# Optimization experiments

Hardware: AMD Instinct MI355X
Metric: run time of the kernel (lower is better)

Reference implementation:

```python
import jax, jax.numpy as jnp
import numpy as np
import math

V = 32000      # vocab_size
D = 1024       # hidden_dims
T_MAX = 1024   # max_txt_len
L = 4          # n_layers
H = 8          # heads (fixed in CausalMHA)
HD = D // H
B, T = 2, 1024
EPS = 1e-5


def setup_inputs() -> dict:
    key = jax.random.key(0)
    ks = jax.random.split(key, 20)
    s = 0.02
    inp = {
        "x": jax.random.randint(ks[0], (B, T), 0, V, dtype=jnp.int64) if jax.config.read("jax_enable_x64") else jax.random.randint(ks[0], (B, T), 0, V, dtype=jnp.int32),
        "tok_emb": jax.random.normal(ks[1], (V, D), jnp.float32) * s,
        "pos_emb": jax.random.normal(ks[2], (1, T_MAX, D), jnp.float32) * s,
        "ln1_g": jnp.ones((L, D), jnp.float32),
        "ln1_b": jnp.zeros((L, D), jnp.float32),
        "wqkv": jax.random.normal(ks[3], (L, D, 3 * D), jnp.float32) * s,
        "bqkv": jnp.zeros((L, 3 * D), jnp.float32),
        "wo": jax.random.normal(ks[4], (L, D, D), jnp.float32) * s,
        "bo": jnp.zeros((L, D), jnp.float32),
        "ln2_g": jnp.ones((L, D), jnp.float32),
        "ln2_b": jnp.zeros((L, D), jnp.float32),
        "wfc": jax.random.normal(ks[5], (L, D, 4 * D), jnp.float32) * s,   # no bias
        "wfc2": jax.random.normal(ks[6], (L, 4 * D, D), jnp.float32) * s,  # no bias
        "fn_g": jnp.ones((D,), jnp.float32),
        "fn_b": jnp.zeros((D,), jnp.float32),
        "wout": jax.random.normal(ks[7], (D, V), jnp.float32) * s,
        "bout": jnp.zeros((V,), jnp.float32),
    }
    return inp


def _ln(x, g, b):
    mu = jnp.mean(x, axis=-1, keepdims=True)
    var = jnp.var(x, axis=-1, keepdims=True)
    return (x - mu) * jax.lax.rsqrt(var + EPS) * g + b


def _attn(xn, wqkv_l, bqkv_l, wo_l, bo_l):
    Bb, Tt, _ = xn.shape
    qkv = xn @ wqkv_l + bqkv_l                      # [B,T,3D]
    q, k, v = jnp.split(qkv, 3, axis=-1)
    q = q.reshape(Bb, Tt, H, HD)
    k = k.reshape(Bb, Tt, H, HD)
    v = v.reshape(Bb, Tt, H, HD)
    scores = jnp.einsum("bqhd,bkhd->bhqk", q, k) / math.sqrt(HD)
    mask = jnp.triu(jnp.ones((Tt, Tt), bool), k=1)   # True above diagonal
    scores = jnp.where(mask, jnp.float32(-jnp.inf), scores)
    att = jax.nn.softmax(scores, axis=-1)
    out = jnp.einsum("bhqk,bkhd->bqhd", att, v).reshape(Bb, Tt, D)
    return out @ wo_l + bo_l


def reference(x, tok_emb, pos_emb, ln1_g, ln1_b, wqkv, bqkv, wo, bo,
              ln2_g, ln2_b, wfc, wfc2, fn_g, fn_b, wout, bout):
    Tt = x.shape[1]
    h = tok_emb[x] + pos_emb[:, :Tt, :]              # [B,T,D]
    for i in range(L):
        h = h + _attn(_ln(h, ln1_g[i], ln1_b[i]), wqkv[i], bqkv[i], wo[i], bo[i])
        hn = _ln(h, ln2_g[i], ln2_b[i])
        h = h + jax.nn.gelu(hn @ wfc[i], approximate=False) @ wfc2[i]
    h = _ln(h, fn_g, fn_b)
    return h @ wout + bout                           # [B,T,V] logits
```

## Files before the change

### kernel.cpp

```cpp
#include <hip/hip_runtime.h>
#include <math.h>
#include <stdint.h>

#define D_  1024
#define T_  1024
#define H_  8
#define HD_ 128
#define L_  4
#define V_  32000
#define M_  2048

typedef __attribute__((ext_vector_type(4))) float f32x4;
typedef __attribute__((ext_vector_type(4))) short s16x4;
typedef __attribute__((ext_vector_type(8))) short s16x8;
typedef unsigned short u16;

__device__ __forceinline__ u16 f2bf(float f) {
  union { float f; uint32_t u; } c; c.f = f;
  uint32_t r = c.u + 0x7fffu + ((c.u >> 16) & 1u);
  return (u16)(r >> 16);
}
__device__ __forceinline__ float bf2f(u16 h) {
  union { uint32_t u; float f; } c; c.u = ((uint32_t)h) << 16;
  return c.f;
}
__device__ __forceinline__ float gelu_f(float x) {
  return 0.5f * x * (1.0f + erff(x * 0.70710678118654752f));
}

__device__ __forceinline__ void gload16(const u16* g, u16* l) {
  __builtin_amdgcn_global_load_lds(
      (const __attribute__((address_space(1))) void*)(uintptr_t)g,
      (__attribute__((address_space(3))) void*)(uint32_t)(uintptr_t)l,
      16, 0, 0);
}

__device__ __forceinline__ void convT_f32_tile(const float* __restrict__ in,
                                               u16* __restrict__ out,
                                               int ldin, int ldout,
                                               int c0, int r0,
                                               u16 (*tile)[72])
{
  const int t = threadIdx.x;
  const int rr = t >> 2, cs = (t & 3) << 4;
  u16 tmp[16];
  const float* p = in + (size_t)(r0 + rr) * ldin + c0 + cs;
#pragma unroll
  for (int q = 0; q < 4; ++q) {
    f32x4 v = *(const f32x4*)(p + q * 4);
#pragma unroll
    for (int j = 0; j < 4; ++j) tmp[q * 4 + j] = f2bf(v[j]);
  }
  *(s16x8*)&tile[rr][cs]     = *(const s16x8*)tmp;
  *(s16x8*)&tile[rr][cs + 8] = *(const s16x8*)(tmp + 8);
  __syncthreads();
  const int cr = t >> 2, rs = (t & 3) << 4;
  u16 o[16];
#pragma unroll
  for (int j = 0; j < 16; ++j) o[j] = tile[rs + j][cr];
  u16* op = out + (size_t)(c0 + cr) * ldout + r0 + rs;
  *(s16x8*)op       = *(const s16x8*)o;
  *(s16x8*)(op + 8) = *(const s16x8*)(o + 8);
}

__device__ __forceinline__
void ln_row_body(int row, float* __restrict__ hbuf, const float* __restrict__ P,
                 const float* __restrict__ g, const float* __restrict__ b,
                 u16* __restrict__ y, int red, float* red_s)
{
  const int tid = threadIdx.x;
  const size_t i = (size_t)row * D_ + tid * 4;
  f32x4 v = *(const f32x4*)&hbuf[i];
  if (red) {
#pragma unroll
    for (int zp = 0; zp < 4; ++zp) {
      f32x4 p = *(const f32x4*)&P[(size_t)zp * M_ * D_ + i];
      v[0] += p[0]; v[1] += p[1]; v[2] += p[2]; v[3] += p[3];
    }
    *(f32x4*)&hbuf[i] = v;
  }
  float s  = v[0] + v[1] + v[2] + v[3];
  float s2 = v[0]*v[0] + v[1]*v[1] + v[2]*v[2] + v[3]*v[3];
#pragma unroll
  for (int off = 32; off > 0; off >>= 1) {
    s  += __shfl_xor(s, off);
    s2 += __shfl_xor(s2, off);
  }
  if ((tid & 63) == 0) { red_s[tid >> 6] = s; red_s[4 + (tid >> 6)] = s2; }
  __syncthreads();
  s  = red_s[0] + red_s[1] + red_s[2] + red_s[3];
  s2 = red_s[4] + red_s[5] + red_s[6] + red_s[7];
  const float mean = s * (1.0f / D_);
  const float var  = s2 * (1.0f / D_) - mean * mean;
  const float rs   = rsqrtf(var + 1e-5f);
  f32x4 gg = *(const f32x4*)&g[tid * 4];
  f32x4 bb = *(const f32x4*)&b[tid * 4];
  u16 o[4];
#pragma unroll
  for (int j = 0; j < 4; ++j) o[j] = f2bf((v[j] - mean) * rs * gg[j] + bb[j]);
  *(s16x4*)&y[i] = *(const s16x4*)o;
}

__global__ __launch_bounds__(256)
void convT_bf16(const u16* __restrict__ in, u16* __restrict__ out,
                int ldin, int ldout, long inZ, long outZ)
{
  __shared__ __align__(16) u16 tile[64][72];
  const int c0 = blockIdx.x << 6, r0 = blockIdx.y << 6;
  const int t = threadIdx.x;
  const int rr = t >> 2, cs = (t & 3) << 4;
  const u16* p = in + (size_t)blockIdx.z * inZ + (size_t)(r0 + rr) * ldin + c0 + cs;
  s16x8 v0 = *(const s16x8*)(p);
  s16x8 v1 = *(const s16x8*)(p + 8);
  *(s16x8*)&tile[rr][cs]     = v0;
  *(s16x8*)&tile[rr][cs + 8] = v1;
  __syncthreads();
  const int cr = t >> 2, rs = (t & 3) << 4;
  u16 o[16];
#pragma unroll
  for (int j = 0; j < 16; ++j) o[j] = tile[rs + j][cr];
  u16* op = out + (size_t)blockIdx.z * outZ + (size_t)(c0 + cr) * ldout + r0 + rs;
  *(s16x8*)op       = *(const s16x8*)o;
  *(s16x8*)(op + 8) = *(const s16x8*)(o + 8);
}

__global__ __launch_bounds__(256)
void conv4ln_kernel(const float* __restrict__ wqkv_l, const float* __restrict__ wo_l,
                    const float* __restrict__ wfc_l, const float* __restrict__ wfc2_l,
                    u16* __restrict__ Wq, u16* __restrict__ Wo,
                    u16* __restrict__ Wf1, u16* __restrict__ Wf2,
                    float* __restrict__ hbuf, const float* __restrict__ P,
                    const float* __restrict__ g, const float* __restrict__ b,
                    u16* __restrict__ y, int red)
{
  __shared__ __align__(16) u16 tile[64][72];
  int f = blockIdx.x;
  if (f < 2048) { ln_row_body(f, hbuf, P, g, b, y, red, (float*)tile); return; }
  f -= 2048;
  if (f < 768) {
    convT_f32_tile(wqkv_l, Wq, 3 * D_, D_, (f % 48) << 6, (f / 48) << 6, tile);
  } else if (f < 1024) {
    f -= 768;
    convT_f32_tile(wo_l, Wo, D_, D_, (f & 15) << 6, (f >> 4) << 6, tile);
  } else if (f < 2048) {
    f -= 1024;
    convT_f32_tile(wfc_l, Wf1, 4 * D_, D_, (f & 63) << 6, (f >> 6) << 6, tile);
  } else {
    f -= 2048;
    convT_f32_tile(wfc2_l, Wf2, D_, 4 * D_, (f & 15) << 6, (f >> 4) << 6, tile);
  }
}

__global__ __launch_bounds__(256)
void convwout_ln(const float* __restrict__ wout, u16* __restrict__ WoutT,
                 float* __restrict__ hbuf, const float* __restrict__ P,
                 const float* __restrict__ g, const float* __restrict__ b,
                 u16* __restrict__ y)
{
  __shared__ __align__(16) u16 tile[64][72];
  int f = blockIdx.x;
  if (f < 2048) { ln_row_body(f, hbuf, P, g, b, y, 1, (float*)tile); return; }
  f -= 2048;
  convT_f32_tile(wout, WoutT, V_, D_, (f % 500) << 6, (f / 500) << 6, tile);
}

template<int TM, int ACT, int BIAS, int OUT>
__device__ __forceinline__
void gemm2_body(const u16* __restrict__ A, const u16* __restrict__ Bw,
                const float* __restrict__ bias, const float* __restrict__ res,
                void* __restrict__ Cv,
                int K, int lda, int ldb, int ldc, float scale,
                int bx, int by)
{
  constexpr int WN  = (TM == 128) ? 2 : 4;
  constexpr int WNW = 128 / WN;
  constexpr int NJ  = WNW / 16;
  constexpr int AR  = TM / 64;

  const int m0 = bx * TM, n0 = by * 128;
  const int ktiles = K >> 5;

  __shared__ __align__(16) u16 As[2][TM * 32];
  __shared__ __align__(16) u16 Bs[2][128 * 32];

  const int tid = threadIdx.x, lane = tid & 63, wave = tid >> 6;
  const int wm = wave / WN, wn = wave % WN;
  const int l15 = lane & 15, l4 = lane >> 4;
  const int srow = lane >> 2, scol = (lane & 3) << 3;

  f32x4 acc[4][NJ];
  const f32x4 z4 = {0.f, 0.f, 0.f, 0.f};
#pragma unroll
  for (int i = 0; i < 4; ++i)
#pragma unroll
    for (int j = 0; j < NJ; ++j) acc[i][j] = z4;

  auto stage = [&](int kt, int buf) {
    const int kc = (kt << 5) + scol;
#pragma unroll
    for (int r = 0; r < AR; ++r) {
      const int row = r * 64 + wave * 16;
      gload16(A + (size_t)(m0 + row + srow) * lda + kc, &As[buf][row * 32]);
    }
#pragma unroll
    for (int r = 0; r < 2; ++r) {
      const int row = r * 64 + wave * 16;
      gload16(Bw + (size_t)(n0 + row + srow) * ldb + kc, &Bs[buf][row * 32]);
    }
  };

  stage(0, 0);
  __syncthreads();

  for (int kt = 0; kt < ktiles; ++kt) {
    const int buf = kt & 1;
    if (kt + 1 < ktiles) stage(kt + 1, buf ^ 1);
    const u16* ap = &As[buf][(wm * 64 + l15) * 32 + (l4 << 3)];
    const u16* bp = &Bs[buf][(wn * WNW + l15) * 32 + (l4 << 3)];
    s16x8 af[4], bf[NJ];
#pragma unroll
    for (int i = 0; i < 4; ++i) af[i] = *(const s16x8*)(ap + i * (16 * 32));
#pragma unroll
    for (int j = 0; j < NJ; ++j) bf[j] = *(const s16x8*)(bp + j * (16 * 32));
#pragma unroll
    for (int i = 0; i < 4; ++i)
#pragma unroll
      for (int j = 0; j < NJ; ++j)
        acc[i][j] = __builtin_amdgcn_mfma_f32_16x16x32_bf16(af[i], bf[j], acc[i][j], 0, 0, 0);
    __syncthreads();
  }

  float* Cf = (float*)Cv;
  u16*   Ch = (u16*)Cv;
#pragma unroll
  for (int i = 0; i < 4; ++i) {
    const int row0 = m0 + wm * 64 + i * 16 + l4 * 4;
#pragma unroll
    for (int j = 0; j < NJ; ++j) {
      const int col = n0 + wn * WNW + j * 16 + l15;
      const float bv = BIAS ? bias[col] : 0.0f;
#pragma unroll
      for (int r = 0; r < 4; ++r) {
        float v = acc[i][j][r] * scale + bv;
        if (ACT) v = gelu_f(v);
        const size_t idx = (size_t)(row0 + r) * ldc + col;
        if (OUT == 0)      Ch[idx] = f2bf(v);
        else if (OUT == 1) Cf[idx] = v;
        else               Cf[idx] = v + res[idx];
      }
    }
  }
}

__device__ __forceinline__ int2 swz2d() {
  const int gx = gridDim.x, gy = gridDim.y;
  int flat = blockIdx.y * gx + blockIdx.x;
  const int nwg = gx * gy;
  int swz = (flat & 7) * (nwg >> 3) + (flat >> 3);
  return make_int2(swz % gx, swz / gx);
}

__global__ __launch_bounds__(256)
void gemm_qkv(const u16* A, const u16* Bw, const float* bias, void* Cv) {
  int2 b = swz2d();
  gemm2_body<128, 0, 1, 0>(A, Bw, bias, nullptr, Cv, D_, D_, D_, 3 * D_, 1.0f, b.x, b.y);
}
__global__ __launch_bounds__(256)
void gemm_wo(const u16* A, const u16* Bw, const float* bias, const float* res,
             void* Cv) {
  int2 b = swz2d();
  gemm2_body<64, 0, 1, 2>(A, Bw, bias, res, Cv, D_, D_, D_, D_, 1.0f, b.x, b.y);
}

template<int OUT, int ACT>
__device__ __forceinline__
void gemm8n_body(const u16* __restrict__ A, int lda,
                 const u16* __restrict__ Bw, int ldb,
                 void* __restrict__ Cv, int ldc, int bx, int by)
{
  const int m0 = bx << 8, n0 = by << 7;

  __shared__ __align__(16) u16 lds[49152];

  const int tid = threadIdx.x, lane = tid & 63, wave = tid >> 6;
  const int wm = wave >> 1, wn = wave & 1;
  const int l15 = lane & 15, l4 = lane >> 4;

  f32x4 acc[4][4];
  const f32x4 z4 = {0.f, 0.f, 0.f, 0.f};
#pragma unroll
  for (int i = 0; i < 4; ++i)
#pragma unroll
    for (int j = 0; j < 4; ++j) acc[i][j] = z4;

  auto stgA = [&](int buf, int kt, int kh) {
    kt = (kt < 15) ? kt : 15;
    const int slot = buf * 24576 + kh * 8192;
#pragma unroll
    for (int r = 0; r < 2; ++r) {
      const int u = r * 512 + (wave << 6) + lane;
      const int rw = u >> 2, ks = u & 3;
      const int ksw = ks ^ ((rw >> 1) & 3);
      gload16(A + (size_t)(m0 + rw) * lda + (kt << 6) + (kh << 5) + (ksw << 3),
              &lds[slot + r * 4096 + (wave << 9)]);
    }
  };
  auto stgB = [&](int buf, int kt, int kh) {
    kt = (kt < 15) ? kt : 15;
    const int slot = buf * 24576 + 16384 + kh * 4096;
    const int u = (wave << 6) + lane;
    const int rw = u >> 2, ks = u & 3;
    const int ksw = ks ^ ((rw >> 1) & 3);
    gload16(Bw + (size_t)(n0 + rw) * ldb + (kt << 6) + (kh << 5) + (ksw << 3),
            &lds[slot + (wave << 9)]);
  };

  s16x8 af[4], bfr[4];

#define LDABN(bb, kk)                                                         \
  {                                                                           \
    _Pragma("unroll") for (int f = 0; f < 4; ++f) {                           \
      const int rw = wm * 64 + f * 16 + l15;                                  \
      af[f] = *(const s16x8*)&lds[(bb) + (kk) * 8192 + rw * 32 +              \
                                  ((l4 ^ ((rw >> 1) & 3)) << 3)];             \
    }                                                                         \
    _Pragma("unroll") for (int f = 0; f < 4; ++f) {                           \
      const int rn = wn * 64 + f * 16 + l15;                                  \
      bfr[f] = *(const s16x8*)&lds[(bb) + 16384 + (kk) * 4096 + rn * 32 +     \
                                   ((l4 ^ ((rn >> 1) & 3)) << 3)];            \
    }                                                                         \
  }
#define MFMAN()                                                               \
  {                                                                           \
    __builtin_amdgcn_s_barrier();                                             \
    asm volatile("s_waitcnt lgkmcnt(0)" ::: "memory");                        \
    __builtin_amdgcn_sched_barrier(0);                                        \
    __builtin_amdgcn_s_setprio(1);                                            \
    _Pragma("unroll") for (int f = 0; f < 4; ++f)                             \
      _Pragma("unroll") for (int nf = 0; nf < 4; ++nf)                        \
        acc[f][nf] = __builtin_amdgcn_mfma_f32_16x16x32_bf16(                 \
            af[f], bfr[nf], acc[f][nf], 0, 0, 0);                             \
    __builtin_amdgcn_s_setprio(0);                                            \
  }
#define BARN() __builtin_amdgcn_s_barrier()
#define VM6()  asm volatile("s_waitcnt vmcnt(6)" ::: "memory")

  stgA(0, 0, 0); stgB(0, 0, 0);
  stgA(0, 0, 1); stgB(0, 0, 1);
  stgA(1, 1, 0); stgB(1, 1, 0);
  VM6();
  BARN();

  for (int i = 0; i < 8; ++i) {
    const int t = 2 * i;
    LDABN(0, 0);
    stgA(1, t + 1, 1); stgB(1, t + 1, 1);
    MFMAN(); VM6(); BARN();
    LDABN(0, 1);
    stgA(0, t + 2, 0); stgB(0, t + 2, 0);
    MFMAN(); VM6(); BARN();
    LDABN(24576, 0);
    stgA(0, t + 2, 1); stgB(0, t + 2, 1);
    MFMAN(); VM6(); BARN();
    LDABN(24576, 1);
    stgA(1, t + 3, 0); stgB(1, t + 3, 0);
    MFMAN(); VM6(); BARN();
  }
#undef LDABN
#undef MFMAN
#undef BARN
#undef VM6

  float* Cf = (float*)Cv;
  u16*   Ch = (u16*)Cv;
#pragma unroll
  for (int mf = 0; mf < 4; ++mf) {
    const int row0 = m0 + wm * 64 + mf * 16 + l4 * 4;
#pragma unroll
    for (int nf = 0; nf < 4; ++nf) {
      const int col = n0 + wn * 64 + nf * 16 + l15;
#pragma unroll
      for (int r = 0; r < 4; ++r) {
        float v = acc[mf][nf][r];
        if (ACT) v = gelu_f(v);
        const size_t idx = (size_t)(row0 + r) * ldc + col;
        if (OUT == 0) Ch[idx] = f2bf(v);
        else          Cf[idx] = v;
      }
    }
  }
}

__global__ __launch_bounds__(512, 1)
void gemm8n_fc1(const u16* A, const u16* Bw, void* Cv) {
  int flat = blockIdx.x;
  int swz = (flat & 7) * 32 + (flat >> 3);
  gemm8n_body<0, 1>(A, 1024, Bw, 1024, Cv, 4096, swz & 7, swz >> 3);
}
__global__ __launch_bounds__(512, 1)
void gemm8n_fc2(const u16* A, const u16* Bw, float* P) {
  int flat = blockIdx.x;
  int swz = (flat & 7) * 32 + (flat >> 3);
  const int bx = swz & 7, by = (swz >> 3) & 7, z = swz >> 6;
  gemm8n_body<1, 0>(A + z * 1024, 4096, Bw + z * 1024, 4096,
                    P + (size_t)z * M_ * D_, 1024, bx, by);
}

__global__ __launch_bounds__(512, 2)
void gemm8_logits(const u16* __restrict__ A, const u16* __restrict__ Bw,
                  const float* __restrict__ bias, float* __restrict__ C)
{
  int flat = blockIdx.x;
  int swz = (flat & 7) * 125 + (flat >> 3);
  const int bx = swz & 7;
  const int by = swz >> 3;
  const int m0 = bx << 8, n0 = by << 8;

  __shared__ __align__(16) u16 lds[65536];

  const int tid = threadIdx.x, lane = tid & 63, wave = tid >> 6;
  const int wm = wave >> 2, wn = wave & 3;
  const int l15 = lane & 15, l4 = lane >> 4;

  f32x4 acc[8][4];
  const f32x4 z4 = {0.f, 0.f, 0.f, 0.f};
#pragma unroll
  for (int i = 0; i < 8; ++i)
#pragma unroll
    for (int j = 0; j < 4; ++j) acc[i][j] = z4;

  auto stg = [&](const u16* G, int rowbase, int slot, int kt, int kh) {
    kt = (kt < 15) ? kt : 15;
#pragma unroll
    for (int r = 0; r < 2; ++r) {
      const int u = r * 512 + (wave << 6) + lane;
      const int rw = u >> 2, ks = u & 3;
      const int ksw = ks ^ ((rw >> 1) & 3);
      const u16* src = G + (size_t)(rowbase + rw) * 1024 + (kt << 6) + (kh << 5) + (ksw << 3);
      gload16(src, &lds[slot + r * 4096 + (wave << 9)]);
    }
  };

  s16x8 af[4], bfr[4];

#define LDA4(bb, kk, mh)                                                      \
  {                                                                           \
    _Pragma("unroll") for (int f = 0; f < 4; ++f) {                           \
      const int rw = wm * 128 + (mh) * 64 + f * 16 + l15;                     \
      af[f] = *(const s16x8*)&lds[(bb) + (kk) * 8192 + rw * 32 +              \
                                  ((l4 ^ ((rw >> 1) & 3)) << 3)];             \
    }                                                                         \
  }
#define LDB4(bb, kk)                                                          \
  {                                                                           \
    _Pragma("unroll") for (int f = 0; f < 4; ++f) {                           \
      const int rn = wn * 64 + f * 16 + l15;                                  \
      bfr[f] = *(const s16x8*)&lds[(bb) + 16384 + (kk) * 8192 + rn * 32 +     \
                                   ((l4 ^ ((rn >> 1) & 3)) << 3)];            \
    }                                                                         \
  }
#define MFMA16(mh)                                                            \
  {                                                                           \
    __builtin_amdgcn_s_barrier();                                             \
    asm volatile("s_waitcnt lgkmcnt(0)" ::: "memory");                        \
    __builtin_amdgcn_sched_barrier(0);                                        \
    __builtin_amdgcn_s_setprio(1);                                            \
    _Pragma("unroll") for (int f = 0; f < 4; ++f)                             \
      _Pragma("unroll") for (int nf = 0; nf < 4; ++nf)                        \
        acc[(mh) * 4 + f][nf] = __builtin_amdgcn_mfma_f32_16x16x32_bf16(      \
            af[f], bfr[nf], acc[(mh) * 4 + f][nf], 0, 0, 0);                  \
    __builtin_amdgcn_s_setprio(0);                                            \
  }
#define BAR() __builtin_amdgcn_s_barrier()
#define VM4() asm volatile("s_waitcnt vmcnt(4)" ::: "memory")

  stg(A,  m0, 0,             0, 0);
  stg(Bw, n0, 16384,         0, 0);
  stg(A,  m0, 8192,          0, 1);
  stg(Bw, n0, 16384 + 8192,  0, 1);
  stg(A,  m0, 32768,         1, 0);
  stg(Bw, n0, 32768 + 16384, 1, 0);
  VM4();
  BAR();

  for (int i = 0; i < 8; ++i) {
    const int t = 2 * i;
    LDA4(0, 0, 0); LDB4(0, 0);
    stg(A, m0, 32768 + 8192, t + 1, 1);
    MFMA16(0); BAR();
    LDA4(0, 0, 1);
    stg(Bw, n0, 32768 + 24576, t + 1, 1);
    MFMA16(1); BAR();
    LDA4(0, 1, 0); LDB4(0, 1);
    stg(A, m0, 0, t + 2, 0);
    MFMA16(0); BAR();
    LDA4(0, 1, 1);
    stg(Bw, n0, 16384, t + 2, 0);
    MFMA16(1); VM4(); BAR();
    LDA4(32768, 0, 0); LDB4(32768, 0);
    stg(A, m0, 8192, t + 2, 1);
    MFMA16(0); BAR();
    LDA4(32768, 0, 1);
    stg(Bw, n0, 16384 + 8192, t + 2, 1);
    MFMA16(1); BAR();
    LDA4(32768, 1, 0); LDB4(32768, 1);
    stg(A, m0, 32768, t + 3, 0);
    MFMA16(0); BAR();
    LDA4(32768, 1, 1);
    stg(Bw, n0, 32768 + 16384, t + 3, 0);
    MFMA16(1); VM4(); BAR();
  }
#undef LDA4
#undef LDB4
#undef MFMA16
#undef BAR
#undef VM4

  float bv[4];
#pragma unroll
  for (int nf = 0; nf < 4; ++nf) bv[nf] = bias[n0 + wn * 64 + nf * 16 + l15];
#pragma unroll
  for (int mf = 0; mf < 8; ++mf) {
    const int row0 = m0 + wm * 128 + mf * 16 + l4 * 4;
#pragma unroll
    for (int nf = 0; nf < 4; ++nf) {
      const int col = n0 + wn * 64 + nf * 16 + l15;
#pragma unroll
      for (int r = 0; r < 4; ++r)
        C[(size_t)(row0 + r) * V_ + col] = acc[mf][nf][r] + bv[nf];
    }
  }
}

__global__ __launch_bounds__(128)
void flash_attn(const u16* __restrict__ qkv, const u16* __restrict__ Vt,
                u16* __restrict__ xo)
{
  int flat = blockIdx.x;
  int swz = (flat & 7) * 64 + (flat >> 3);
  const int qb = 31 - (swz & 31);
  const int z  = swz >> 5;
  const int b  = z >> 3, hh = z & 7;

  __shared__ __align__(16) u16 Ks[64 * 128];
  __shared__ __align__(16) u16 Vs[128 * 64];
  __shared__ __align__(16) u16 Ps[32 * 80];

  const int tid = threadIdx.x, lane = tid & 63, w = tid >> 6;
  const int l15 = lane & 15, l4 = lane >> 4;
  const float iscale = 0.08838834764831845f;

  const int qrow = qb * 32 + w * 16 + l15;
  const u16* qptr = qkv + ((size_t)(b * T_) + qrow) * (3 * D_) + hh * HD_;

  s16x8 bQ[4];
#pragma unroll
  for (int ks = 0; ks < 4; ++ks)
    bQ[ks] = *(const s16x8*)(qptr + ks * 32 + l4 * 8);

  f32x4 O[8];
#pragma unroll
  for (int i = 0; i < 8; ++i) O[i] = {0.f, 0.f, 0.f, 0.f};
  float m_run = -1e30f, l_run = 0.f;

  const int ntiles = (qb >> 1) + 1;
  for (int kt = 0; kt < ntiles; ++kt) {
    __syncthreads();
    {
      const int r = tid >> 1, c0 = (tid & 1) << 6;
      const u16* src = qkv + ((size_t)(b * T_) + kt * 64 + r) * (3 * D_) + D_ + hh * HD_ + c0;
#pragma unroll
      for (int u = 0; u < 8; ++u) {
        s16x8 v = *(const s16x8*)(src + u * 8);
        const int dblk = (c0 >> 3) + u;
        *(s16x8*)&Ks[r * 128 + ((dblk ^ (r & 7)) << 3)] = v;
      }
      const int d = tid;
      const u16* vsrc = Vt + ((size_t)z * HD_ + d) * T_ + kt * 64;
#pragma unroll
      for (int u = 0; u < 8; ++u) {
        s16x8 v = *(const s16x8*)(vsrc + u * 8);
        *(s16x8*)&Vs[d * 64 + ((u ^ (d & 7)) << 3)] = v;
      }
    }
    __syncthreads();

    f32x4 st[4];
#pragma unroll
    for (int mf = 0; mf < 4; ++mf) st[mf] = {0.f, 0.f, 0.f, 0.f};
#pragma unroll
    for (int ks = 0; ks < 4; ++ks) {
      s16x8 aK[4];
#pragma unroll
      for (int mf = 0; mf < 4; ++mf) {
        const int r = mf * 16 + l15;
        aK[mf] = *(const s16x8*)&Ks[r * 128 + ((((ks << 2) + l4) ^ (r & 7)) << 3)];
      }
#pragma unroll
      for (int mf = 0; mf < 4; ++mf)
        st[mf] = __builtin_amdgcn_mfma_f32_16x16x32_bf16(aK[mf], bQ[ks], st[mf], 0, 0, 0);
    }

    const bool diag = (kt == ntiles - 1);
    float sv[16];
    float mx = -1e30f;
#pragma unroll
    for (int mf = 0; mf < 4; ++mf)
#pragma unroll
      for (int r = 0; r < 4; ++r) {
        float s = st[mf][r] * iscale;
        if (diag) {
          const int k = kt * 64 + mf * 16 + l4 * 4 + r;
          if (k > qrow) s = -1e30f;
        }
        sv[mf * 4 + r] = s;
        mx = fmaxf(mx, s);
      }
    mx = fmaxf(mx, __shfl_xor(mx, 16));
    mx = fmaxf(mx, __shfl_xor(mx, 32));
    const float m_new = fmaxf(m_run, mx);
    const float sc_old = __expf(m_run - m_new);
    float psum = 0.f;
    u16 pb[16];
#pragma unroll
    for (int j = 0; j < 16; ++j) {
      const float p = __expf(sv[j] - m_new);
      psum += p;
      pb[j] = f2bf(p);
    }
    psum += __shfl_xor(psum, 16);
    psum += __shfl_xor(psum, 32);
    l_run = l_run * sc_old + psum;
    m_run = m_new;

    float scr[4];
#pragma unroll
    for (int r = 0; r < 4; ++r) scr[r] = __shfl(sc_old, l4 * 4 + r);
#pragma unroll
    for (int df = 0; df < 8; ++df)
#pragma unroll
      for (int r = 0; r < 4; ++r) O[df][r] *= scr[r];

    {
      const int row = w * 16 + l15;
#pragma unroll
      for (int j = 0; j < 16; ++j) {
        const int k = (j >> 2) * 16 + l4 * 4 + (j & 3);
        Ps[row * 80 + (((k >> 3) ^ (l15 & 7)) << 3) + (k & 7)] = pb[j];
      }
    }

#pragma unroll
    for (int kc = 0; kc < 2; ++kc) {
      const int prow = w * 16 + l15;
      s16x8 aP = *(const s16x8*)&Ps[prow * 80 + ((((kc << 2) + l4) ^ (l15 & 7)) << 3)];
#pragma unroll
      for (int df = 0; df < 8; ++df) {
        const int d = df * 16 + l15;
        s16x8 bV = *(const s16x8*)&Vs[d * 64 + ((((kc << 2) + l4) ^ (d & 7)) << 3)];
        O[df] = __builtin_amdgcn_mfma_f32_16x16x32_bf16(aP, bV, O[df], 0, 0, 0);
      }
    }
  }

  const float inv_l = 1.0f / l_run;
  float invr[4];
#pragma unroll
  for (int r = 0; r < 4; ++r) invr[r] = __shfl(inv_l, l4 * 4 + r);
#pragma unroll
  for (int df = 0; df < 8; ++df)
#pragma unroll
    for (int r = 0; r < 4; ++r) {
      const int row = qb * 32 + w * 16 + l4 * 4 + r;
      xo[((size_t)(b * T_) + row) * D_ + hh * HD_ + df * 16 + l15] =
          f2bf(O[df][r] * invr[r]);
    }
}

__global__ __launch_bounds__(256)
void ln_bf16(const float* __restrict__ x, const float* __restrict__ g,
             const float* __restrict__ b, u16* __restrict__ y)
{
  __shared__ float red_s[8];
  ln_row_body(blockIdx.x, (float*)x, nullptr, g, b, y, 0, red_s);
}

__global__ __launch_bounds__(256)
void embed_kernel(const int* __restrict__ x, const float* __restrict__ tok,
                  const float* __restrict__ pos, float* __restrict__ h)
{
  const int row = blockIdx.x, tid = threadIdx.x;
  const int t = row & (T_ - 1);
  const int id = x[row];
  f32x4 a = *(const f32x4*)&tok[(size_t)id * D_ + tid * 4];
  f32x4 p = *(const f32x4*)&pos[(size_t)t * D_ + tid * 4];
  f32x4 o = {a[0] + p[0], a[1] + p[1], a[2] + p[2], a[3] + p[3]};
  *(f32x4*)&h[(size_t)row * D_ + tid * 4] = o;
}

extern "C" void kernel_launch(void* const* d_in, const int* in_sizes, int n_in,
                              void* d_out, int out_size, void* d_ws, size_t ws_size,
                              hipStream_t stream)
{
  (void)in_sizes; (void)n_in; (void)out_size; (void)ws_size;
  const int*   x     = (const int*)  d_in[0];
  const float* tok   = (const float*)d_in[1];
  const float* pos   = (const float*)d_in[2];
  const float* ln1_g = (const float*)d_in[3];
  const float* ln1_b = (const float*)d_in[4];
  const float* wqkv  = (const float*)d_in[5];
  const float* bqkv  = (const float*)d_in[6];
  const float* wo    = (const float*)d_in[7];
  const float* bo    = (const float*)d_in[8];
  const float* ln2_g = (const float*)d_in[9];
  const float* ln2_b = (const float*)d_in[10];
  const float* wfc   = (const float*)d_in[11];
  const float* wfc2  = (const float*)d_in[12];
  const float* fn_g  = (const float*)d_in[13];
  const float* fn_b  = (const float*)d_in[14];
  const float* wout  = (const float*)d_in[15];
  const float* bout  = (const float*)d_in[16];
  float* out = (float*)d_out;

  float* h  = (float*)d_ws;
  u16* xn   = (u16*)(h + (size_t)M_ * D_);
  u16* Wq   = xn  + (size_t)M_ * D_;
  u16* Wo   = Wq  + (size_t)3 * D_ * D_;
  u16* Wf1  = Wo  + (size_t)D_ * D_;
  u16* Wf2  = Wf1 + (size_t)4 * D_ * D_;
  u16* qkv  = Wf2 + (size_t)4 * D_ * D_;
  u16* Vt   = qkv + (size_t)M_ * 3 * D_;
  u16* S    = Vt  + (size_t)2 * T_ * D_;
  float* P  = (float*)(S + (size_t)M_ * 4 * D_);
  u16* WoutT = Wq;

  embed_kernel<<<M_, 256, 0, stream>>>(x, tok, pos, h);

  for (int l = 0; l < L_; ++l) {
    conv4ln_kernel<<<5120, 256, 0, stream>>>(
        wqkv + (size_t)l * D_ * 3 * D_, wo + (size_t)l * D_ * D_,
        wfc + (size_t)l * D_ * 4 * D_, wfc2 + (size_t)l * 4 * D_ * D_,
        Wq, Wo, Wf1, Wf2,
        h, P, ln1_g + l * D_, ln1_b + l * D_, xn, l > 0 ? 1 : 0);
    gemm_qkv<<<dim3(16, 24), 256, 0, stream>>>(xn, Wq, bqkv + l * 3 * D_, qkv);
    convT_bf16<<<dim3(16, 16, 2), 256, 0, stream>>>(
        qkv + 2 * D_, Vt, 3 * D_, T_, (long)T_ * 3 * D_, (long)T_ * D_);
    flash_attn<<<512, 128, 0, stream>>>(qkv, Vt, xn);
    gemm_wo<<<dim3(32, 8), 256, 0, stream>>>(xn, Wo, bo + l * D_, h, h);
    ln_bf16<<<M_, 256, 0, stream>>>(h, ln2_g + l * D_, ln2_b + l * D_, xn);
    gemm8n_fc1<<<256, 512, 0, stream>>>(xn, Wf1, S);
    gemm8n_fc2<<<256, 512, 0, stream>>>(S, Wf2, P);
  }

  convwout_ln<<<10048, 256, 0, stream>>>(wout, WoutT, h, P, fn_g, fn_b, xn);
  gemm8_logits<<<1000, 512, 0, stream>>>(xn, WoutT, bout, out);
}
```

Measured before the change: 880.8 us.

## Fuse V transpose into QKV GEMM epilogue and split-K Wo GEMM with LN fold

The QKV GEMM epilogue now writes the V columns directly in transposed layout, which removes the separate convT_bf16 kernel. The QKV tile height drops to 64 to double the workgroup count. The Wo projection becomes a split-K GEMM over two K halves with 512 workgroups, writing fp32 partials. A new ln_fold2 kernel adds both partials, the bias and the residual, then applies LN2, replacing the residual add in the old Wo epilogue and the separate ln_bf16 launch. The cost is extra fp32 partial traffic and a scattered 4-element transposed store pattern for V.

```diff
diff --git a/kernel.cpp b/kernel.cpp
--- a/kernel.cpp
+++ b/kernel.cpp
@@ -99,29 +99,6 @@
 #pragma unroll
   for (int j = 0; j < 4; ++j) o[j] = f2bf((v[j] - mean) * rs * gg[j] + bb[j]);
   *(s16x4*)&y[i] = *(const s16x4*)o;
-}
-
-__global__ __launch_bounds__(256)
-void convT_bf16(const u16* __restrict__ in, u16* __restrict__ out,
-                int ldin, int ldout, long inZ, long outZ)
-{
-  __shared__ __align__(16) u16 tile[64][72];
-  const int c0 = blockIdx.x << 6, r0 = blockIdx.y << 6;
-  const int t = threadIdx.x;
-  const int rr = t >> 2, cs = (t & 3) << 4;
-  const u16* p = in + (size_t)blockIdx.z * inZ + (size_t)(r0 + rr) * ldin + c0 + cs;
-  s16x8 v0 = *(const s16x8*)(p);
-  s16x8 v1 = *(const s16x8*)(p + 8);
-  *(s16x8*)&tile[rr][cs]     = v0;
-  *(s16x8*)&tile[rr][cs + 8] = v1;
-  __syncthreads();
-  const int cr = t >> 2, rs = (t & 3) << 4;
-  u16 o[16];
-#pragma unroll
-  for (int j = 0; j < 16; ++j) o[j] = tile[rs + j][cr];
-  u16* op = out + (size_t)blockIdx.z * outZ + (size_t)(c0 + cr) * ldout + r0 + rs;
-  *(s16x8*)op       = *(const s16x8*)o;
-  *(s16x8*)(op + 8) = *(const s16x8*)(o + 8);
 }
 
 __global__ __launch_bounds__(256)
@@ -164,13 +141,50 @@
   convT_f32_tile(wout, WoutT, V_, D_, (f % 500) << 6, (f / 500) << 6, tile);
 }
 
-template<int TM, int ACT, int BIAS, int OUT>
+__global__ __launch_bounds__(256)
+void ln_fold2(float* __restrict__ hbuf, const float* __restrict__ P,
+              const float* __restrict__ bo, const float* __restrict__ g,
+              const float* __restrict__ b, u16* __restrict__ y)
+{
+  __shared__ float red_s[8];
+  const int row = blockIdx.x, tid = threadIdx.x;
+  const size_t i = (size_t)row * D_ + tid * 4;
+  f32x4 v  = *(const f32x4*)&hbuf[i];
+  f32x4 p0 = *(const f32x4*)&P[i];
+  f32x4 p1 = *(const f32x4*)&P[(size_t)M_ * D_ + i];
+  f32x4 bb4 = *(const f32x4*)&bo[tid * 4];
+#pragma unroll
+  for (int j = 0; j < 4; ++j) v[j] += p0[j] + p1[j] + bb4[j];
+  *(f32x4*)&hbuf[i] = v;
+  float s  = v[0] + v[1] + v[2] + v[3];
+  float s2 = v[0]*v[0] + v[1]*v[1] + v[2]*v[2] + v[3]*v[3];
+#pragma unroll
+  for (int off = 32; off > 0; off >>= 1) {
+    s  += __shfl_xor(s, off);
+    s2 += __shfl_xor(s2, off);
+  }
+  if ((tid & 63) == 0) { red_s[tid >> 6] = s; red_s[4 + (tid >> 6)] = s2; }
+  __syncthreads();
+  s  = red_s[0] + red_s[1] + red_s[2] + red_s[3];
+  s2 = red_s[4] + red_s[5] + red_s[6] + red_s[7];
+  const float mean = s * (1.0f / D_);
+  const float var  = s2 * (1.0f / D_) - mean * mean;
+  const float rs   = rsqrtf(var + 1e-5f);
+  f32x4 gg = *(const f32x4*)&g[tid * 4];
+  f32x4 bb = *(const f32x4*)&b[tid * 4];
+  u16 o[4];
+#pragma unroll
+  for (int j = 0; j < 4; ++j) o[j] = f2bf((v[j] - mean) * rs * gg[j] + bb[j]);
+  *(s16x4*)&y[i] = *(const s16x4*)o;
+}
+
+template<int TM, int ACT, int BIAS, int OUT, int VSPLIT>
 __device__ __forceinline__
 void gemm2_body(const u16* __restrict__ A, const u16* __restrict__ Bw,
                 const float* __restrict__ bias, const float* __restrict__ res,
                 void* __restrict__ Cv,
                 int K, int lda, int ldb, int ldc, float scale,
-                int bx, int by)
+                int bx, int by, u16* __restrict__ VtOut)
 {
   constexpr int WN  = (TM == 128) ? 2 : 4;
   constexpr int WNW = 128 / WN;
@@ -239,14 +253,27 @@
     for (int j = 0; j < NJ; ++j) {
       const int col = n0 + wn * WNW + j * 16 + l15;
       const float bv = BIAS ? bias[col] : 0.0f;
+      float vv[4];
 #pragma unroll
       for (int r = 0; r < 4; ++r) {
         float v = acc[i][j][r] * scale + bv;
         if (ACT) v = gelu_f(v);
-        const size_t idx = (size_t)(row0 + r) * ldc + col;
-        if (OUT == 0)      Ch[idx] = f2bf(v);
-        else if (OUT == 1) Cf[idx] = v;
-        else               Cf[idx] = v + res[idx];
+        vv[r] = v;
+      }
+      if (VSPLIT && col >= 2048) {
+        u16 o4[4];
+#pragma unroll
+        for (int r = 0; r < 4; ++r) o4[r] = f2bf(vv[r]);
+        const int bb = row0 >> 10, t0 = row0 & 1023, c2 = col - 2048;
+        *(s16x4*)&VtOut[((size_t)(bb << 10) + c2) * 1024 + t0] = *(const s16x4*)o4;
+      } else {
+#pragma unroll
+        for (int r = 0; r < 4; ++r) {
+          const size_t idx = (size_t)(row0 + r) * ldc + col;
+          if (OUT == 0)      Ch[idx] = f2bf(vv[r]);
+          else if (OUT == 1) Cf[idx] = vv[r];
+          else               Cf[idx] = vv[r] + res[idx];
+        }
       }
     }
   }
@@ -261,15 +288,24 @@
 }
 
 __global__ __launch_bounds__(256)
-void gemm_qkv(const u16* A, const u16* Bw, const float* bias, void* Cv) {
+void gemm_qkv(const u16* A, const u16* Bw, const float* bias, void* Cv, u16* Vt) {
   int2 b = swz2d();
-  gemm2_body<128, 0, 1, 0>(A, Bw, bias, nullptr, Cv, D_, D_, D_, 3 * D_, 1.0f, b.x, b.y);
+  gemm2_body<64, 0, 1, 0, 1>(A, Bw, bias, nullptr, Cv, D_, D_, D_, 3 * D_, 1.0f,
+                             b.x, b.y, Vt);
 }
 __global__ __launch_bounds__(256)
-void gemm_wo(const u16* A, const u16* Bw, const float* bias, const float* res,
-             void* Cv) {
-  int2 b = swz2d();
-  gemm2_body<64, 0, 1, 2>(A, Bw, bias, res, Cv, D_, D_, D_, D_, 1.0f, b.x, b.y);
+void gemm_wo_s(const u16* __restrict__ A, const u16* __restrict__ Bw,
+               float* __restrict__ P) {
+  const int gx = gridDim.x, gy = gridDim.y;
+  int flat = (blockIdx.z * gy + blockIdx.y) * gx + blockIdx.x;
+  const int nwg = gx * gy * gridDim.z;
+  int swz = (flat & 7) * (nwg >> 3) + (flat >> 3);
+  const int bx = swz % gx; swz /= gx;
+  const int by = swz % gy;
+  const int z  = swz / gy;
+  gemm2_body<64, 0, 0, 1, 0>(A + z * 512, Bw + z * 512, nullptr, nullptr,
+                             P + (size_t)z * M_ * D_,
+                             512, D_, D_, D_, 1.0f, bx, by, nullptr);
 }
 
 template<int OUT, int ACT>
@@ -678,14 +714,6 @@
 }
 
 __global__ __launch_bounds__(256)
-void ln_bf16(const float* __restrict__ x, const float* __restrict__ g,
-             const float* __restrict__ b, u16* __restrict__ y)
-{
-  __shared__ float red_s[8];
-  ln_row_body(blockIdx.x, (float*)x, nullptr, g, b, y, 0, red_s);
-}
-
-__global__ __launch_bounds__(256)
 void embed_kernel(const int* __restrict__ x, const float* __restrict__ tok,
                   const float* __restrict__ pos, float* __restrict__ h)
 {
@@ -742,12 +770,11 @@
         wfc + (size_t)l * D_ * 4 * D_, wfc2 + (size_t)l * 4 * D_ * D_,
         Wq, Wo, Wf1, Wf2,
         h, P, ln1_g + l * D_, ln1_b + l * D_, xn, l > 0 ? 1 : 0);
-    gemm_qkv<<<dim3(16, 24), 256, 0, stream>>>(xn, Wq, bqkv + l * 3 * D_, qkv);
-    convT_bf16<<<dim3(16, 16, 2), 256, 0, stream>>>(
-        qkv + 2 * D_, Vt, 3 * D_, T_, (long)T_ * 3 * D_, (long)T_ * D_);
+    gemm_qkv<<<dim3(32, 24), 256, 0, stream>>>(xn, Wq, bqkv + l * 3 * D_, qkv, Vt);
     flash_attn<<<512, 128, 0, stream>>>(qkv, Vt, xn);
-    gemm_wo<<<dim3(32, 8), 256, 0, stream>>>(xn, Wo, bo + l * D_, h, h);
-    ln_bf16<<<M_, 256, 0, stream>>>(h, ln2_g + l * D_, ln2_b + l * D_, xn);
+    gemm_wo_s<<<dim3(32, 8, 2), 256, 0, stream>>>(xn, Wo, P);
+    ln_fold2<<<M_, 256, 0, stream>>>(h, P, bo + l * D_,
+                                     ln2_g + l * D_, ln2_b + l * D_, xn);
     gemm8n_fc1<<<256, 512, 0, stream>>>(xn, Wf1, S);
     gemm8n_fc2<<<256, 512, 0, stream>>>(S, Wf2, P);
   }
```

Result: faster. 841.6 us (-4.4%).
